# Performance work log

Hardware: AMD Instinct MI355X
Metric: run time of the kernel (lower is better)

## Reference

```python
import jax, jax.numpy as jnp
import numpy as np
import math

B, S, DIM = 2, 2048, 2048
H, HD, RD = 16, 128, 64
LKV, LQ = 512, 1536

def _rope(x, cos, sin):
    # x: (B,S,H,RD); interpret consecutive pairs as complex, multiply by e^{i theta}
    b, s, h, d = x.shape
    xr = x.reshape(b, s, h, d // 2, 2)
    xre, xim = xr[..., 0], xr[..., 1]
    c = cos[None, :, None, :]  # (1,S,1,d/2)
    sn = sin[None, :, None, :]
    ore = xre * c - xim * sn
    oim = xre * sn + xim * c
    return jnp.stack([ore, oim], axis=-1).reshape(b, s, h, d)

def setup_inputs() -> dict:
    key = jax.random.key(0)
    ks = jax.random.split(key, 12)
    def w(k, shape, fan_in):
        return jax.random.normal(k, shape, jnp.float32) * (1.0 / math.sqrt(fan_in))
    x = jax.random.normal(ks[0], (B, S, DIM), jnp.float32)
    # RoPE tables for decoupled rotary subspace of width RD
    inv_freq = 1.0 / (10000.0 ** (np.arange(0, RD, 2, dtype=np.float32) / RD))
    ang = np.outer(np.arange(S, dtype=np.float32), inv_freq)  # (S, RD/2)
    freq_cos = jnp.asarray(np.cos(ang), jnp.float32)
    freq_sin = jnp.asarray(np.sin(ang), jnp.float32)
    return {
        "x": x, "freq_cos": freq_cos, "freq_sin": freq_sin,
        "Wkv": w(ks[1], (DIM, LKV), DIM),          # latent_kv (no bias)
        "Wlq": w(ks[2], (DIM, LQ), DIM),           # latent_q (no bias)
        "Wq": w(ks[3], (LQ, H * HD), LQ),          # query (no bias)
        "Wk": w(ks[4], (LKV, H * HD), LKV),        # key (no bias)
        "Wv": w(ks[5], (LKV, H * HD), LKV),        # value (no bias)
        "Wqr": w(ks[6], (LQ, H * RD), LQ),         # decop_rot_q (bias=True)
        "bqr": jnp.zeros((H * RD,), jnp.float32),
        "Wkr": w(ks[7], (DIM, H * RD), DIM),       # decop_rot_k (bias=True)
        "bkr": jnp.zeros((H * RD,), jnp.float32),
        "Wo": w(ks[8], (H * HD, DIM), H * HD),     # out_proj (bias=True)
        "bo": jnp.zeros((DIM,), jnp.float32),
    }

def reference(x, freq_cos, freq_sin, Wkv, Wlq, Wq, Wk, Wv, Wqr, bqr, Wkr, bkr, Wo, bo):
    b, s, _ = x.shape
    cq = x @ Wlq                      # (B,S,LQ)
    ckv = x @ Wkv                     # (B,S,LKV)
    q = (cq @ Wq).reshape(b, s, H, HD)
    qr = _rope((cq @ Wqr + bqr).reshape(b, s, H, RD), freq_cos, freq_sin)
    k = (ckv @ Wk).reshape(b, s, H, HD)
    kr = _rope((x @ Wkr + bkr).reshape(b, s, H, RD), freq_cos, freq_sin)
    v = (ckv @ Wv).reshape(b, s, H, HD)
    qf = jnp.concatenate([q, qr], axis=-1)   # (B,S,H,HD+RD)
    kf = jnp.concatenate([k, kr], axis=-1)
    scale = 1.0 / math.sqrt(HD + RD)
    scores = jnp.einsum('bqhd,bkhd->bhqk', qf, kf) * scale
    # masked=True path: causal tril mask over full seq_len
    mask = jnp.tril(jnp.ones((s, s), bool))
    scores = jnp.where(mask[None, None], scores, -jnp.inf)
    att = jax.nn.softmax(scores.astype(jnp.float32), axis=-1).astype(qf.dtype)
    out = jnp.einsum('bhqk,bkhd->bqhd', att, v).reshape(b, s, H * HD)
    return out @ Wo + bo
```

## Files before the change

kernel.cpp:

```cpp
#include <hip/hip_runtime.h>
#include <hip/hip_bf16.h>
#include <stdint.h>

#define S_LEN 2048
#define NB 2
#define NH 16
#define HDIM 128
#define RDIM 64
#define DF 192
#define MROWS 4096

typedef __bf16 bf16_t;
typedef __attribute__((ext_vector_type(8))) __bf16 bf16x8;
typedef __attribute__((ext_vector_type(4))) __bf16 bf16x4;
typedef __attribute__((ext_vector_type(4))) float f32x4;
typedef __attribute__((ext_vector_type(4))) float float4v;

__device__ __forceinline__ void gload_lds16(const bf16_t* g, bf16_t* l) {
  __builtin_amdgcn_global_load_lds(
      (const __attribute__((address_space(1))) void*)g,
      (__attribute__((address_space(3))) void*)l, 16, 0, 0);
}

__global__ __launch_bounds__(256) void convert_bf16(const float* __restrict__ in,
                                                    bf16_t* __restrict__ out, int n4) {
  int i = blockIdx.x * 256 + threadIdx.x;
  if (i >= n4) return;
  float4v v = *reinterpret_cast<const float4v*>(&in[(size_t)i * 4]);
  bf16x4 o;
  o[0] = (bf16_t)v[0]; o[1] = (bf16_t)v[1]; o[2] = (bf16_t)v[2]; o[3] = (bf16_t)v[3];
  *reinterpret_cast<bf16x4*>(&out[(size_t)i * 4]) = o;
}

struct TrDesc { const float* src; bf16_t* dst; int K; int N; int nbx; int base; };
struct TrPack { TrDesc d[8]; };

__global__ __launch_bounds__(256) void transpose_all(TrPack p) {
  __shared__ float t[64][65];
  const int bid = blockIdx.x;
  int m = 0;
#pragma unroll
  for (int i = 1; i < 8; ++i) m += (bid >= p.d[i].base);
  const TrDesc td = p.d[m];
  const int local = bid - td.base;
  const int n0 = (local % td.nbx) * 64, k0 = (local / td.nbx) * 64;
  const int tx = threadIdx.x & 63, ty = threadIdx.x >> 6;
#pragma unroll
  for (int i = ty; i < 64; i += 4)
    t[i][tx] = td.src[(size_t)(k0 + i) * td.N + n0 + tx];
  __syncthreads();
#pragma unroll
  for (int i = ty; i < 64; i += 4)
    td.dst[(size_t)(n0 + i) * td.K + k0 + tx] = (bf16_t)t[tx][i];
}

struct EpiParams {
  bf16_t* o0;
  bf16_t* o1;
  bf16_t* o2;
  float* outf;
  const float* bias;
  const float* cosb;
  const float* sinb;
};

template <int MODE>
__device__ __forceinline__ void gemm_body(const bf16_t* __restrict__ A,
                                          const bf16_t* __restrict__ Bt,
                                          int N, int K, int m0, int n0,
                                          bf16_t (*Ab)[256 * 64],
                                          bf16_t (*Bb)[128 * 64], EpiParams ep) {
  const int tid = threadIdx.x;
  const int lane = tid & 63, w = tid >> 6;
  const int l15 = lane & 15, lg = lane >> 4;
  const int mw = (w >> 1) * 64, nw = (w & 1) * 64;
  const int nt = K >> 6;

  auto stageA = [&](int t, int buf, int j) {
    const int s = j * 512 + tid;
    const int row = s >> 3, c = s & 7;
    const int cs = c ^ (row & 7);
    gload_lds16(A + (size_t)(m0 + row) * K + (t << 6) + cs * 8, &Ab[buf][s * 8]);
  };
  auto stageB = [&](int t, int buf, int j) {
    const int s = j * 512 + tid;
    const int row = s >> 3, c = s & 7;
    const int cs = c ^ (row & 7);
    gload_lds16(Bt + (size_t)(n0 + row) * K + (t << 6) + cs * 8, &Bb[buf][s * 8]);
  };

  f32x4 acc[4][4] = {};
#pragma unroll
  for (int j = 0; j < 4; ++j) stageA(0, 0, j);
#pragma unroll
  for (int j = 0; j < 2; ++j) stageB(0, 0, j);
  asm volatile("s_waitcnt vmcnt(0)" ::: "memory");
  __builtin_amdgcn_s_barrier();

  for (int t = 0; t < nt; ++t) {
    const int cur = t & 1;
    const bool pf = (t + 1 < nt);
    bf16x8 a[4], b[4];
#pragma unroll
    for (int p = 0; p < 4; ++p) {
      const int kk = p >> 1, ih = p & 1;
      const int c = kk * 4 + lg;
      if (ih == 0) {
#pragma unroll
        for (int i = 0; i < 4; ++i) {
          const int r = mw + i * 16 + l15;
          a[i] = *reinterpret_cast<const bf16x8*>(&Ab[cur][r * 64 + ((c ^ (r & 7)) << 3)]);
        }
#pragma unroll
        for (int j = 0; j < 2; ++j) {
          const int r = nw + j * 16 + l15;
          b[j] = *reinterpret_cast<const bf16x8*>(&Bb[cur][r * 64 + ((c ^ (r & 7)) << 3)]);
        }
      } else {
#pragma unroll
        for (int j = 2; j < 4; ++j) {
          const int r = nw + j * 16 + l15;
          b[j] = *reinterpret_cast<const bf16x8*>(&Bb[cur][r * 64 + ((c ^ (r & 7)) << 3)]);
        }
      }
      if (pf) {
        if (p == 0) { stageA(t + 1, cur ^ 1, 0); stageA(t + 1, cur ^ 1, 1); stageA(t + 1, cur ^ 1, 2); }
        if (p == 1) { stageA(t + 1, cur ^ 1, 3); stageB(t + 1, cur ^ 1, 0); stageB(t + 1, cur ^ 1, 1); }
        if (p == 3) asm volatile("s_waitcnt vmcnt(0)" ::: "memory");
      }
      __builtin_amdgcn_s_barrier();
      asm volatile("s_waitcnt lgkmcnt(0)" ::: "memory");
      __builtin_amdgcn_sched_barrier(0);
      __builtin_amdgcn_s_setprio(1);
      if (ih == 0) {
#pragma unroll
        for (int i = 0; i < 4; ++i)
#pragma unroll
          for (int j = 0; j < 2; ++j)
            acc[i][j] = __builtin_amdgcn_mfma_f32_16x16x32_bf16(a[i], b[j], acc[i][j], 0, 0, 0);
      } else {
#pragma unroll
        for (int i = 0; i < 4; ++i)
#pragma unroll
          for (int j = 2; j < 4; ++j)
            acc[i][j] = __builtin_amdgcn_mfma_f32_16x16x32_bf16(a[i], b[j], acc[i][j], 0, 0, 0);
      }
      __builtin_amdgcn_s_setprio(0);
      __builtin_amdgcn_s_barrier();
    }
  }

#pragma unroll
  for (int i = 0; i < 4; ++i)
#pragma unroll
    for (int j = 0; j < 4; ++j) {
      const int col = n0 + nw + j * 16 + l15;
#pragma unroll
      for (int r = 0; r < 4; ++r) {
        const int row = m0 + mw + i * 16 + lg * 4 + r;
        float v = acc[i][j][r];
        const int b = row >> 11, s = row & 2047;
        if constexpr (MODE == 1) {
          ep.outf[(size_t)row * N + col] = v + ep.bias[col];
        } else if constexpr (MODE == 5) {
          if (col < 1536) {
            ep.o0[(size_t)row * 1536 + col] = (bf16_t)v;
          } else if (col < 2048) {
            ep.o1[(size_t)row * 512 + (col - 1536)] = (bf16_t)v;
          } else {
            const int c2 = col - 2048;
            float vb = v + ep.bias[c2];
            float other = __shfl_xor(vb, 1, 64);
            const int h = c2 >> 6, dr = c2 & 63;
            const int fi = dr >> 1;
            const float c = ep.cosb[s * 32 + fi];
            const float sn = ep.sinb[s * 32 + fi];
            const float o = (c2 & 1) ? (other * sn + vb * c) : (vb * c - other * sn);
            ep.o2[(((size_t)(b * NH + h)) * S_LEN + s) * DF + 128 + dr] = (bf16_t)o;
          }
        } else if constexpr (MODE == 6) {
          if (col < 2048) {
            const int h = col >> 7, d = col & 127;
            ep.o0[(((size_t)(b * NH + h)) * S_LEN + s) * DF + d] = (bf16_t)v;
          } else {
            const int c2 = col - 2048;
            float vb = v + ep.bias[c2];
            float other = __shfl_xor(vb, 1, 64);
            const int h = c2 >> 6, dr = c2 & 63;
            const int fi = dr >> 1;
            const float c = ep.cosb[s * 32 + fi];
            const float sn = ep.sinb[s * 32 + fi];
            const float o = (c2 & 1) ? (other * sn + vb * c) : (vb * c - other * sn);
            ep.o0[(((size_t)(b * NH + h)) * S_LEN + s) * DF + 128 + dr] = (bf16_t)o;
          }
        } else {
          if (col < 2048) {
            const int h = col >> 7, d = col & 127;
            ep.o0[(((size_t)(b * NH + h)) * S_LEN + s) * DF + d] = (bf16_t)v;
          } else {
            const int c2 = col - 2048;
            const int h = c2 >> 7, d = c2 & 127;
            ep.o1[(((size_t)(b * NH + h)) * HDIM + d) * S_LEN + s] = (bf16_t)v;
          }
        }
      }
    }
}

template <int MODE>
__global__ __launch_bounds__(512, 2) void gemm_4p(const bf16_t* __restrict__ A,
                                                  const bf16_t* __restrict__ Bt,
                                                  int N, int K, EpiParams ep) {
  __shared__ alignas(16) bf16_t Ab[2][256 * 64];
  __shared__ alignas(16) bf16_t Bb[2][128 * 64];
  const int nwg = gridDim.x;
  int f = blockIdx.x;
  f = (f & 7) * (nwg >> 3) + (f >> 3);
  const int nbx = N >> 7;
  const int m0 = (f / nbx) * 256, n0 = (f % nbx) * 128;
  gemm_body<MODE>(A, Bt, N, K, m0, n0, Ab, Bb, ep);
}

__global__ __launch_bounds__(512, 2) void gemm_4p67(const bf16_t* __restrict__ A6,
                                                    const bf16_t* __restrict__ Bt6,
                                                    const bf16_t* __restrict__ A7,
                                                    const bf16_t* __restrict__ Bt7,
                                                    EpiParams ep6, EpiParams ep7) {
  __shared__ alignas(16) bf16_t Ab[2][256 * 64];
  __shared__ alignas(16) bf16_t Bb[2][128 * 64];
  const int bid = blockIdx.x;
  if (bid < 384) {
    int f = (bid & 7) * 48 + (bid >> 3);
    const int m0 = (f / 24) * 256, n0 = (f % 24) * 128;
    gemm_body<6>(A6, Bt6, 3072, 1536, m0, n0, Ab, Bb, ep6);
  } else {
    int b2 = bid - 384;
    int f = (b2 & 7) * 64 + (b2 >> 3);
    const int m0 = (f / 32) * 256, n0 = (f % 32) * 128;
    gemm_body<7>(A7, Bt7, 4096, 512, m0, n0, Ab, Bb, ep7);
  }
}

__global__ __launch_bounds__(256, 2) void attn_fwd(const bf16_t* __restrict__ qf,
                                                   const bf16_t* __restrict__ kf,
                                                   const bf16_t* __restrict__ vT,
                                                   bf16_t* __restrict__ att) {
  const int tid = threadIdx.x;
  const int lane = tid & 63, w = tid >> 6;
  const int l15 = lane & 15, lg = lane >> 4;
  const int l = blockIdx.x;
  const int bh = (l & 7) * 4 + ((l >> 3) & 3);
  const int qchunk = l >> 5;
  const int qb0 = (15 - qchunk) * 128;
  const int q0 = qb0 + w * 32;
  const float scale = 0.07216878364870322f;

  __shared__ alignas(16) bf16_t Ks[64 * 192];
  __shared__ alignas(16) bf16_t Vs[128 * 64];
  __shared__ alignas(16) bf16_t Ps[4 * 2048];

  bf16x8 qfr[2][6];
#pragma unroll
  for (int mf = 0; mf < 2; ++mf) {
    const bf16_t* qptr = qf + ((size_t)bh * S_LEN + q0 + mf * 16 + l15) * DF + lg * 8;
#pragma unroll
    for (int d = 0; d < 6; ++d)
      qfr[mf][d] = *reinterpret_cast<const bf16x8*>(qptr + d * 32);
  }

  f32x4 o[2][8] = {};
  float mrun[2] = {-1e30f, -1e30f}, lsum[2] = {0.0f, 0.0f};

  const bf16_t* kb0 = kf + (size_t)bh * S_LEN * DF;
  const bf16_t* vb0 = vT + (size_t)bh * HDIM * S_LEN;
  const int njt = qb0 / 64 + 2;
  const int wslot = tid & ~63;

  for (int jt = 0; jt < njt; ++jt) {
    const int j0 = jt * 64;
    __syncthreads();
    const bf16_t* kTile = kb0 + (size_t)j0 * DF;
#pragma unroll
    for (int i = 0; i < 6; ++i) {
      const int s = i * 256 + tid;
      const int row = s / 24;
      const int c = s - row * 24;
      const int cs = c ^ (row & 7);
      gload_lds16(kTile + (size_t)row * DF + cs * 8,
                  Ks + (size_t)(i * 256 + wslot) * 8);
    }
    const bf16_t* vTile = vb0 + j0;
#pragma unroll
    for (int i = 0; i < 4; ++i) {
      const int s = i * 256 + tid;
      const int row = s >> 3;
      const int c = s & 7;
      const int cs = c ^ (row & 7);
      gload_lds16(vTile + (size_t)row * S_LEN + cs * 8,
                  Vs + (size_t)(i * 256 + wslot) * 8);
    }
    __syncthreads();

    if (j0 > q0 + 31) continue;

    f32x4 sa[2][4] = {};
    __builtin_amdgcn_s_setprio(1);
#pragma unroll
    for (int jf = 0; jf < 4; ++jf) {
      const int krow = jf * 16 + l15;
      const int ksw = krow & 7;
#pragma unroll
      for (int d = 0; d < 6; ++d) {
        const int kc = (4 * d + lg) ^ ksw;
        bf16x8 kfr = *reinterpret_cast<const bf16x8*>(&Ks[krow * 192 + kc * 8]);
#pragma unroll
        for (int mf = 0; mf < 2; ++mf)
          sa[mf][jf] =
              __builtin_amdgcn_mfma_f32_16x16x32_bf16(kfr, qfr[mf][d], sa[mf][jf], 0, 0, 0);
      }
    }
    __builtin_amdgcn_s_setprio(0);

#pragma unroll
    for (int mf = 0; mf < 2; ++mf) {
      const int qi = q0 + mf * 16 + l15;
      const bool full = (j0 + 63 <= q0 + mf * 16);
      float sv[16];
#pragma unroll
      for (int jf = 0; jf < 4; ++jf)
#pragma unroll
        for (int r = 0; r < 4; ++r) {
          float x = sa[mf][jf][r] * scale;
          if (!full) {
            const int j = j0 + jf * 16 + lg * 4 + r;
            if (j > qi) x = -1e30f;
          }
          sv[jf * 4 + r] = x;
        }

      float a8[8];
#pragma unroll
      for (int i = 0; i < 8; ++i) a8[i] = fmaxf(sv[i], sv[i + 8]);
#pragma unroll
      for (int i = 0; i < 4; ++i) a8[i] = fmaxf(a8[i], a8[i + 4]);
      float mx = fmaxf(fmaxf(a8[0], a8[1]), fmaxf(a8[2], a8[3]));
      mx = fmaxf(mx, __shfl_xor(mx, 16, 64));
      mx = fmaxf(mx, __shfl_xor(mx, 32, 64));

      if (__any(mx > mrun[mf] + 8.0f)) {
        const float mn = fmaxf(mrun[mf], mx);
        const float alpha = __expf(mrun[mf] - mn);
        mrun[mf] = mn;
        lsum[mf] *= alpha;
        float af[4];
#pragma unroll
        for (int r = 0; r < 4; ++r) af[r] = __shfl(alpha, lg * 4 + r, 16);
#pragma unroll
        for (int dt = 0; dt < 8; ++dt)
#pragma unroll
          for (int r = 0; r < 4; ++r) o[mf][dt][r] *= af[r];
      }

#pragma unroll
      for (int i = 0; i < 16; ++i) sv[i] = __expf(sv[i] - mrun[mf]);
      float s8[8];
#pragma unroll
      for (int i = 0; i < 8; ++i) s8[i] = sv[i] + sv[i + 8];
#pragma unroll
      for (int i = 0; i < 4; ++i) s8[i] = s8[i] + s8[i + 4];
      float sm = (s8[0] + s8[1]) + (s8[2] + s8[3]);
      sm += __shfl_xor(sm, 16, 64);
      sm += __shfl_xor(sm, 32, 64);
      lsum[mf] += sm;

#pragma unroll
      for (int jf = 0; jf < 4; ++jf) {
        bf16x4 pk;
#pragma unroll
        for (int r = 0; r < 4; ++r) pk[r] = (bf16_t)sv[jf * 4 + r];
        const int key = jf * 16 + lg * 4;
        *reinterpret_cast<bf16x4*>(
            &Ps[w * 2048 + mf * 1024 + l15 * 64 + (key ^ ((l15 & 7) << 3))]) = pk;
      }
    }
    asm volatile("s_waitcnt lgkmcnt(0)" ::: "memory");
    __builtin_amdgcn_sched_barrier(0);
    bf16x8 pfr[2][2];
#pragma unroll
    for (int mf = 0; mf < 2; ++mf)
#pragma unroll
      for (int jk = 0; jk < 2; ++jk)
        pfr[mf][jk] = *reinterpret_cast<const bf16x8*>(
            &Ps[w * 2048 + mf * 1024 + l15 * 64 + (((jk * 4 + lg) ^ (l15 & 7)) << 3)]);

    __builtin_amdgcn_s_setprio(1);
#pragma unroll
    for (int dt = 0; dt < 8; ++dt) {
      const int vrow = dt * 16 + l15;
      const int vsw = vrow & 7;
#pragma unroll
      for (int jk = 0; jk < 2; ++jk) {
        const int vc = (jk * 4 + lg) ^ vsw;
        bf16x8 vfr = *reinterpret_cast<const bf16x8*>(&Vs[vrow * 64 + vc * 8]);
#pragma unroll
        for (int mf = 0; mf < 2; ++mf)
          o[mf][dt] =
              __builtin_amdgcn_mfma_f32_16x16x32_bf16(pfr[mf][jk], vfr, o[mf][dt], 0, 0, 0);
      }
    }
    __builtin_amdgcn_s_setprio(0);
  }

  const int b = bh >> 4, h = bh & 15;
#pragma unroll
  for (int mf = 0; mf < 2; ++mf) {
    const float inv = 1.0f / lsum[mf];
    float iv[4];
#pragma unroll
    for (int r = 0; r < 4; ++r) iv[r] = __shfl(inv, lg * 4 + r, 16);
#pragma unroll
    for (int dt = 0; dt < 8; ++dt)
#pragma unroll
      for (int r = 0; r < 4; ++r) {
        const int s = q0 + mf * 16 + lg * 4 + r;
        att[((size_t)b * S_LEN + s) * 2048 + h * 128 + dt * 16 + l15] =
            (bf16_t)(o[mf][dt][r] * iv[r]);
      }
  }
}

extern "C" void kernel_launch(void* const* d_in, const int* in_sizes, int n_in,
                              void* d_out, int out_size, void* d_ws, size_t ws_size,
                              hipStream_t stream) {
  const float* x    = (const float*)d_in[0];
  const float* fcos = (const float*)d_in[1];
  const float* fsin = (const float*)d_in[2];
  const float* Wkv  = (const float*)d_in[3];
  const float* Wlq  = (const float*)d_in[4];
  const float* Wq   = (const float*)d_in[5];
  const float* Wk   = (const float*)d_in[6];
  const float* Wv   = (const float*)d_in[7];
  const float* Wqr  = (const float*)d_in[8];
  const float* bqr  = (const float*)d_in[9];
  const float* Wkr  = (const float*)d_in[10];
  const float* bkr  = (const float*)d_in[11];
  const float* Wo   = (const float*)d_in[12];
  const float* bo   = (const float*)d_in[13];
  float* out = (float*)d_out;

  char* ws = (char*)d_ws;
  size_t off = 0;
  auto alloc = [&](size_t bytes) {
    void* p = ws + off;
    off += (bytes + 255) & ~(size_t)255;
    return p;
  };
  bf16_t* xb    = (bf16_t*)alloc((size_t)MROWS * 2048 * 2);
  bf16_t* WcatA = (bf16_t*)alloc((size_t)3072 * 2048 * 2);
  bf16_t* WcatB = (bf16_t*)alloc((size_t)3072 * 1536 * 2);
  bf16_t* WcatC = (bf16_t*)alloc((size_t)4096 * 512 * 2);
  bf16_t* WoT   = (bf16_t*)alloc((size_t)2048 * 2048 * 2);
  bf16_t* cq    = (bf16_t*)alloc((size_t)MROWS * 1536 * 2);
  bf16_t* ckv   = (bf16_t*)alloc((size_t)MROWS * 512 * 2);
  bf16_t* qfb   = (bf16_t*)alloc((size_t)NB * NH * S_LEN * DF * 2);
  bf16_t* kfb   = (bf16_t*)alloc((size_t)NB * NH * S_LEN * DF * 2);
  bf16_t* vTb   = (bf16_t*)alloc((size_t)NB * NH * HDIM * S_LEN * 2);
  bf16_t* attb  = (bf16_t*)alloc((size_t)MROWS * 2048 * 2);

  {
    int n4 = (MROWS * 2048) / 4;
    convert_bf16<<<dim3((n4 + 255) / 256), dim3(256), 0, stream>>>(x, xb, n4);
  }
  {
    TrPack p;
    int base = 0;
    auto set = [&](int i, const float* s, bf16_t* d, int K, int N) {
      p.d[i] = {s, d, K, N, N / 64, base};
      base += (N / 64) * (K / 64);
    };
    set(0, Wlq, WcatA, 2048, 1536);
    set(1, Wkv, WcatA + (size_t)1536 * 2048, 2048, 512);
    set(2, Wkr, WcatA + (size_t)2048 * 2048, 2048, 1024);
    set(3, Wq,  WcatB, 1536, 2048);
    set(4, Wqr, WcatB + (size_t)2048 * 1536, 1536, 1024);
    set(5, Wk,  WcatC, 512, 2048);
    set(6, Wv,  WcatC + (size_t)2048 * 512, 512, 2048);
    set(7, Wo,  WoT, 2048, 2048);
    transpose_all<<<dim3(base), dim3(256), 0, stream>>>(p);
  }

  EpiParams ep{}, ep2{};

  ep = {cq, ckv, kfb, nullptr, bkr, fcos, fsin};
  gemm_4p<5><<<dim3(384), dim3(512), 0, stream>>>(xb, WcatA, 3072, 2048, ep);
  ep  = {qfb, nullptr, nullptr, nullptr, bqr, fcos, fsin};
  ep2 = {kfb, vTb, nullptr, nullptr, nullptr, nullptr, nullptr};
  gemm_4p67<<<dim3(896), dim3(512), 0, stream>>>(cq, WcatB, ckv, WcatC, ep, ep2);
  attn_fwd<<<dim3(512), dim3(256), 0, stream>>>(qfb, kfb, vTb, attb);
  ep = {nullptr, nullptr, nullptr, out, bo, nullptr, nullptr};
  gemm_4p<1><<<dim3(256), dim3(512), 0, stream>>>(attb, WoT, 2048, 2048, ep);
}
```

Baseline: 375.5 us.

## Enlarge GEMM tiles to 256x256 with 2x4 wave layout per block

Grows each GEMM workgroup's output tile from 256x128 to 256x256. The 8 waves are rearranged so each computes a 128x64 sub-tile with 32 accumulators, B fragments are loaded once per k-step, and A fragments are streamed per phase. This raises arithmetic intensity and halves global reloads of A, but halves the grid (the out-projection GEMM drops to 128 blocks, fewer than the CU count) and doubles LDS and accumulator register use, which can reduce occupancy.

```diff
diff --git a/kernel.cpp b/kernel.cpp
--- a/kernel.cpp
+++ b/kernel.cpp
@@ -69,89 +69,82 @@
                                           const bf16_t* __restrict__ Bt,
                                           int N, int K, int m0, int n0,
                                           bf16_t (*Ab)[256 * 64],
-                                          bf16_t (*Bb)[128 * 64], EpiParams ep) {
+                                          bf16_t (*Bb)[256 * 64], EpiParams ep) {
   const int tid = threadIdx.x;
   const int lane = tid & 63, w = tid >> 6;
   const int l15 = lane & 15, lg = lane >> 4;
-  const int mw = (w >> 1) * 64, nw = (w & 1) * 64;
+  const int mw = (w >> 2) * 128, nw = (w & 3) * 64;
   const int nt = K >> 6;
 
-  auto stageA = [&](int t, int buf, int j) {
-    const int s = j * 512 + tid;
+  auto stage = [&](int t, int buf, int j) {
+    const int s = (j & 3) * 512 + tid;
     const int row = s >> 3, c = s & 7;
     const int cs = c ^ (row & 7);
-    gload_lds16(A + (size_t)(m0 + row) * K + (t << 6) + cs * 8, &Ab[buf][s * 8]);
+    if (j < 4)
+      gload_lds16(A + (size_t)(m0 + row) * K + (t << 6) + cs * 8, &Ab[buf][s * 8]);
+    else
+      gload_lds16(Bt + (size_t)(n0 + row) * K + (t << 6) + cs * 8, &Bb[buf][s * 8]);
   };
-  auto stageB = [&](int t, int buf, int j) {
-    const int s = j * 512 + tid;
-    const int row = s >> 3, c = s & 7;
-    const int cs = c ^ (row & 7);
-    gload_lds16(Bt + (size_t)(n0 + row) * K + (t << 6) + cs * 8, &Bb[buf][s * 8]);
-  };
-
-  f32x4 acc[4][4] = {};
-#pragma unroll
-  for (int j = 0; j < 4; ++j) stageA(0, 0, j);
-#pragma unroll
-  for (int j = 0; j < 2; ++j) stageB(0, 0, j);
+
+  f32x4 acc[8][4] = {};
+#pragma unroll
+  for (int j = 0; j < 8; ++j) stage(0, 0, j);
   asm volatile("s_waitcnt vmcnt(0)" ::: "memory");
   __builtin_amdgcn_s_barrier();
 
   for (int t = 0; t < nt; ++t) {
     const int cur = t & 1;
     const bool pf = (t + 1 < nt);
-    bf16x8 a[4], b[4];
+    bf16x8 bfrag[4][2];
 #pragma unroll
     for (int p = 0; p < 4; ++p) {
-      const int kk = p >> 1, ih = p & 1;
-      const int c = kk * 4 + lg;
-      if (ih == 0) {
-#pragma unroll
-        for (int i = 0; i < 4; ++i) {
-          const int r = mw + i * 16 + l15;
-          a[i] = *reinterpret_cast<const bf16x8*>(&Ab[cur][r * 64 + ((c ^ (r & 7)) << 3)]);
+      if (p == 0) {
+#pragma unroll
+        for (int j = 0; j < 4; ++j)
+#pragma unroll
+          for (int kk = 0; kk < 2; ++kk) {
+            const int r = nw + j * 16 + l15;
+            const int c = kk * 4 + lg;
+            bfrag[j][kk] = *reinterpret_cast<const bf16x8*>(
+                &Bb[cur][r * 64 + ((c ^ (r & 7)) << 3)]);
+          }
+      }
+      bf16x8 afrag[2][2];
+#pragma unroll
+      for (int di = 0; di < 2; ++di)
+#pragma unroll
+        for (int kk = 0; kk < 2; ++kk) {
+          const int r = mw + (p * 2 + di) * 16 + l15;
+          const int c = kk * 4 + lg;
+          afrag[di][kk] = *reinterpret_cast<const bf16x8*>(
+              &Ab[cur][r * 64 + ((c ^ (r & 7)) << 3)]);
         }
-#pragma unroll
-        for (int j = 0; j < 2; ++j) {
-          const int r = nw + j * 16 + l15;
-          b[j] = *reinterpret_cast<const bf16x8*>(&Bb[cur][r * 64 + ((c ^ (r & 7)) << 3)]);
-        }
-      } else {
-#pragma unroll
-        for (int j = 2; j < 4; ++j) {
-          const int r = nw + j * 16 + l15;
-          b[j] = *reinterpret_cast<const bf16x8*>(&Bb[cur][r * 64 + ((c ^ (r & 7)) << 3)]);
-        }
-      }
       if (pf) {
-        if (p == 0) { stageA(t + 1, cur ^ 1, 0); stageA(t + 1, cur ^ 1, 1); stageA(t + 1, cur ^ 1, 2); }
-        if (p == 1) { stageA(t + 1, cur ^ 1, 3); stageB(t + 1, cur ^ 1, 0); stageB(t + 1, cur ^ 1, 1); }
-        if (p == 3) asm volatile("s_waitcnt vmcnt(0)" ::: "memory");
-      }
+        if (p == 0) { stage(t + 1, cur ^ 1, 0); stage(t + 1, cur ^ 1, 1);
+                      stage(t + 1, cur ^ 1, 2); stage(t + 1, cur ^ 1, 3); }
+        if (p == 1) { stage(t + 1, cur ^ 1, 4); stage(t + 1, cur ^ 1, 5);
+                      stage(t + 1, cur ^ 1, 6); stage(t + 1, cur ^ 1, 7); }
+      }
+      if (p == 3) asm volatile("s_waitcnt vmcnt(0)" ::: "memory");
       __builtin_amdgcn_s_barrier();
       asm volatile("s_waitcnt lgkmcnt(0)" ::: "memory");
       __builtin_amdgcn_sched_barrier(0);
       __builtin_amdgcn_s_setprio(1);
-      if (ih == 0) {
-#pragma unroll
-        for (int i = 0; i < 4; ++i)
-#pragma unroll
-          for (int j = 0; j < 2; ++j)
-            acc[i][j] = __builtin_amdgcn_mfma_f32_16x16x32_bf16(a[i], b[j], acc[i][j], 0, 0, 0);
-      } else {
-#pragma unroll
-        for (int i = 0; i < 4; ++i)
-#pragma unroll
-          for (int j = 2; j < 4; ++j)
-            acc[i][j] = __builtin_amdgcn_mfma_f32_16x16x32_bf16(a[i], b[j], acc[i][j], 0, 0, 0);
-      }
+#pragma unroll
+      for (int kk = 0; kk < 2; ++kk)
+#pragma unroll
+        for (int di = 0; di < 2; ++di)
+#pragma unroll
+          for (int j = 0; j < 4; ++j)
+            acc[p * 2 + di][j] = __builtin_amdgcn_mfma_f32_16x16x32_bf16(
+                afrag[di][kk], bfrag[j][kk], acc[p * 2 + di][j], 0, 0, 0);
       __builtin_amdgcn_s_setprio(0);
       __builtin_amdgcn_s_barrier();
     }
   }
 
 #pragma unroll
-  for (int i = 0; i < 4; ++i)
+  for (int i = 0; i < 8; ++i)
 #pragma unroll
     for (int j = 0; j < 4; ++j) {
       const int col = n0 + nw + j * 16 + l15;
@@ -208,35 +201,35 @@
 }
 
 template <int MODE>
-__global__ __launch_bounds__(512, 2) void gemm_4p(const bf16_t* __restrict__ A,
+__global__ __launch_bounds__(512, 2) void gemm_t8(const bf16_t* __restrict__ A,
                                                   const bf16_t* __restrict__ Bt,
                                                   int N, int K, EpiParams ep) {
   __shared__ alignas(16) bf16_t Ab[2][256 * 64];
-  __shared__ alignas(16) bf16_t Bb[2][128 * 64];
+  __shared__ alignas(16) bf16_t Bb[2][256 * 64];
   const int nwg = gridDim.x;
   int f = blockIdx.x;
   f = (f & 7) * (nwg >> 3) + (f >> 3);
-  const int nbx = N >> 7;
-  const int m0 = (f / nbx) * 256, n0 = (f % nbx) * 128;
+  const int nbx = N >> 8;
+  const int m0 = (f / nbx) * 256, n0 = (f % nbx) * 256;
   gemm_body<MODE>(A, Bt, N, K, m0, n0, Ab, Bb, ep);
 }
 
-__global__ __launch_bounds__(512, 2) void gemm_4p67(const bf16_t* __restrict__ A6,
+__global__ __launch_bounds__(512, 2) void gemm_t867(const bf16_t* __restrict__ A6,
                                                     const bf16_t* __restrict__ Bt6,
                                                     const bf16_t* __restrict__ A7,
                                                     const bf16_t* __restrict__ Bt7,
                                                     EpiParams ep6, EpiParams ep7) {
   __shared__ alignas(16) bf16_t Ab[2][256 * 64];
-  __shared__ alignas(16) bf16_t Bb[2][128 * 64];
+  __shared__ alignas(16) bf16_t Bb[2][256 * 64];
   const int bid = blockIdx.x;
-  if (bid < 384) {
-    int f = (bid & 7) * 48 + (bid >> 3);
-    const int m0 = (f / 24) * 256, n0 = (f % 24) * 128;
+  if (bid < 192) {
+    int f = (bid & 7) * 24 + (bid >> 3);
+    const int m0 = (f / 12) * 256, n0 = (f % 12) * 256;
     gemm_body<6>(A6, Bt6, 3072, 1536, m0, n0, Ab, Bb, ep6);
   } else {
-    int b2 = bid - 384;
-    int f = (b2 & 7) * 64 + (b2 >> 3);
-    const int m0 = (f / 32) * 256, n0 = (f % 32) * 128;
+    int b2 = bid - 192;
+    int f = (b2 & 7) * 32 + (b2 >> 3);
+    const int m0 = (f / 16) * 256, n0 = (f % 16) * 256;
     gemm_body<7>(A7, Bt7, 4096, 512, m0, n0, Ab, Bb, ep7);
   }
 }
@@ -492,11 +485,11 @@
   EpiParams ep{}, ep2{};
 
   ep = {cq, ckv, kfb, nullptr, bkr, fcos, fsin};
-  gemm_4p<5><<<dim3(384), dim3(512), 0, stream>>>(xb, WcatA, 3072, 2048, ep);
+  gemm_t8<5><<<dim3(192), dim3(512), 0, stream>>>(xb, WcatA, 3072, 2048, ep);
   ep  = {qfb, nullptr, nullptr, nullptr, bqr, fcos, fsin};
   ep2 = {kfb, vTb, nullptr, nullptr, nullptr, nullptr, nullptr};
-  gemm_4p67<<<dim3(896), dim3(512), 0, stream>>>(cq, WcatB, ckv, WcatC, ep, ep2);
+  gemm_t867<<<dim3(448), dim3(512), 0, stream>>>(cq, WcatB, ckv, WcatC, ep, ep2);
   attn_fwd<<<dim3(512), dim3(256), 0, stream>>>(qfb, kfb, vTb, attb);
   ep = {nullptr, nullptr, nullptr, out, bo, nullptr, nullptr};
-  gemm_4p<1><<<dim3(256), dim3(512), 0, stream>>>(attb, WoT, 2048, 2048, ep);
-}
+  gemm_t8<1><<<dim3(128), dim3(512), 0, stream>>>(attb, WoT, 2048, 2048, ep);
+}
```

Result: no change. 380.7 us (+1.4%).
